# Kernel optimization log

Hardware: AMD Instinct MI355X
Metric: run time of the kernel (lower is better)

The kernel has to match this reference:

```python
import jax, jax.numpy as jnp
import numpy as np

B, N, F, L, H, C = 128, 512, 128, 64, 128, 10

def setup_inputs() -> dict:
    key = jax.random.key(0)
    ks = jax.random.split(key, 20)
    s = 0.1
    return {
        "g": jax.random.uniform(ks[0], (B, N, N), dtype=jnp.float32) + 1e-3,
        "h": jax.random.normal(ks[1], (B, N, F), dtype=jnp.float32),
        "labels": jax.random.randint(ks[2], (B,), 0, C),
        "eps": jax.random.normal(ks[3], (B, N, 1), dtype=jnp.float32),
        "W_s": jax.random.normal(ks[4], (F, L), dtype=jnp.float32) * s,
        "b_s": jnp.zeros((L,), jnp.float32),
        "W_mu": jax.random.normal(ks[5], (L, 1), dtype=jnp.float32) * s,
        "b_mu": jnp.zeros((1,), jnp.float32),
        "W_lv": jax.random.normal(ks[6], (L, 1), dtype=jnp.float32) * s,
        "b_lv": jnp.zeros((1,), jnp.float32),
        "W_dec": jax.random.normal(ks[7], (1, L), dtype=jnp.float32) * s,
        "b_dec": jnp.zeros((L,), jnp.float32),
        "W1": jax.random.normal(ks[8], (L, H), dtype=jnp.float32) * s,
        "b1": jnp.zeros((H,), jnp.float32),
        "W2": jax.random.normal(ks[9], (H, C), dtype=jnp.float32) * s,
        "b2": jnp.zeros((C,), jnp.float32),
        "beta": jnp.array([50.0], jnp.float32),
    }

def _gcn(gn, x, W, b):
    # GCN layer: propagate then project then ELU activation (dropout = 0)
    return jax.nn.elu(jnp.einsum('bnm,bmf->bnf', gn, x) @ W + b)

def reference(g, h, labels, eps, W_s, b_s, W_mu, b_mu, W_lv, b_lv, W_dec, b_dec, W1, b1, W2, b2, beta):
    # norm_g: degrees = sum over dim 1; broadcast division normalizes COLUMNS
    # (torch g/degrees with degrees of shape [N] divides g[:, j] by degrees[j])
    deg = jnp.sum(g, axis=1)                      # [B, N]
    gn = g / deg[:, None, :]                      # column-normalized adjacency
    h1 = _gcn(gn, h, W_s, b_s)                    # [B, N, L]
    mu = _gcn(gn, h1, W_mu, b_mu)                 # [B, N, 1]
    lv = _gcn(gn, h1, W_lv, b_lv)                 # [B, N, 1]
    z = mu + eps * jnp.exp(0.5 * lv)              # reparameterize (training)
    v = jax.nn.sigmoid(beta[0] * z)               # [B, N, 1]
    d = _gcn(gn, v, W_dec, b_dec)                 # [B, N, L]
    hp = jnp.einsum('bnl,bn->bl', h1, v[..., 0])  # h.T @ v pooling -> [B, L]
    logits = jax.nn.log_softmax(jax.nn.elu(hp @ W1 + b1) @ W2 + b2, axis=1)
    nll = -jnp.mean(logits[jnp.arange(B), labels])
    mus = mu.reshape(-1, 1)
    lvs = lv.reshape(-1, 1)
    M = mus.shape[0]
    kl = (-0.5 / M) * jnp.mean(jnp.sum(1.0 + 2.0 * lvs - mus**2 - jnp.exp(lvs)**2, axis=1))
    mse = jnp.mean((h1 - d) ** 2)
    loss = nll + kl + mse
    acc = jnp.mean((jnp.argmax(logits, axis=1) == labels).astype(jnp.float32))
    return (loss, acc)
```

## Files before the change

kernel.cpp:

```cpp
#include <hip/hip_runtime.h>

#define B_  128
#define N_  512
#define F_  128
#define L_  64
#define H_  128
#define C_  10

typedef short  bf8_t  __attribute__((ext_vector_type(8)));
typedef float  f32x4  __attribute__((ext_vector_type(4)));
typedef unsigned short us8 __attribute__((ext_vector_type(8)));

static __device__ __forceinline__ unsigned short f2bf(float x) {
    union { float f; unsigned u; } c; c.f = x;
    unsigned r = (c.u + 0x7fffu + ((c.u >> 16) & 1u)) >> 16;
    return (unsigned short)r;
}
static __device__ __forceinline__ float bf2f(unsigned short s) {
    union { unsigned u; float f; } c; c.u = ((unsigned)s) << 16;
    return c.f;
}
static __device__ __forceinline__ float elu(float x) { return x > 0.f ? x : expm1f(x); }

#define OFF_DEGP   0
#define OFF_DEG    2097152
#define OFF_HPP    2162688
#define OFF_KLP    2228224
#define OFF_MSEP   2229248
#define OFF_V      2230272
#define OFF_LP     2295808
#define OFF_COR    2295936
#define OFF_TMUBF  2296064
#define OFF_TLVBF  2328832
#define OFF_WVBF   2361600
#define OFF_H1Q    2394368
#define OFF_GBF    4491520
#define OFF_UBFT   21268736
#define OFF_WSTBF  23365888

__global__ __launch_bounds__(256) void k1_deg(const float* __restrict__ g,
                                              const float* __restrict__ Ws,
                                              float* __restrict__ deg_part,
                                              unsigned short* __restrict__ gbf,
                                              unsigned short* __restrict__ WsTbf) {
    const int c8 = blockIdx.x, b = blockIdx.y;
    if (c8 == 0 && b == 0) {
        for (int i = threadIdx.x; i < F_ * L_; i += 256) {
            int l = i >> 7, f = i & 127;
            WsTbf[i] = f2bf(Ws[f * L_ + l]);
        }
    }
    const int w = threadIdx.x >> 6, lane = threadIdx.x & 63;
    const int r0 = c8 * 64 + w * 16;
    const float*    gp = g   + ((size_t)b * N_ + r0) * N_ + lane * 8;
    unsigned short* gq = gbf + ((size_t)b * N_ + r0) * N_ + lane * 8;
    float cs[8] = {};
    #pragma unroll 4
    for (int r = 0; r < 16; ++r) {
        float4 v0 = *reinterpret_cast<const float4*>(gp + (size_t)r * N_);
        float4 v1 = *reinterpret_cast<const float4*>(gp + (size_t)r * N_ + 4);
        cs[0] += v0.x; cs[1] += v0.y; cs[2] += v0.z; cs[3] += v0.w;
        cs[4] += v1.x; cs[5] += v1.y; cs[6] += v1.z; cs[7] += v1.w;
        us8 qv;
        qv[0] = f2bf(v0.x); qv[1] = f2bf(v0.y); qv[2] = f2bf(v0.z); qv[3] = f2bf(v0.w);
        qv[4] = f2bf(v1.x); qv[5] = f2bf(v1.y); qv[6] = f2bf(v1.z); qv[7] = f2bf(v1.w);
        *reinterpret_cast<us8*>(gq + (size_t)r * N_) = qv;
    }
    const int s = c8 * 4 + w;
    float* dp = deg_part + ((size_t)(b * 32 + s)) * N_ + lane * 8;
    *reinterpret_cast<float4*>(dp)     = make_float4(cs[0], cs[1], cs[2], cs[3]);
    *reinterpret_cast<float4*>(dp + 4) = make_float4(cs[4], cs[5], cs[6], cs[7]);
}

__global__ __launch_bounds__(256) void k2_u(const float* __restrict__ h,
                                            const unsigned short* __restrict__ WsTbf,
                                            const float* __restrict__ deg_part,
                                            float* __restrict__ deg,
                                            unsigned short* __restrict__ ubfT) {
    __shared__ float tile[64 * 65];
    __shared__ float sdeg[64];
    const int b    = blockIdx.y;
    const int m0   = blockIdx.x * 64;
    const int tid  = threadIdx.x;
    const int wave = tid >> 6, lane = tid & 63;
    const int ml = lane & 15, q = lane >> 4;
    const int row0 = wave * 16;

    if (tid < 64) {
        int j = m0 + tid;
        float s = 0.f;
        #pragma unroll
        for (int k = 0; k < 32; ++k) s += deg_part[(size_t)(b * 32 + k) * N_ + j];
        sdeg[tid] = s;
        deg[b * N_ + j] = s;
    }

    const float* A = h + (size_t)(b * N_ + m0 + row0 + ml) * F_ + q * 8;
    const unsigned short* Bb = WsTbf + ml * F_ + q * 8;

    f32x4 acc[4] = {};
    #pragma unroll
    for (int kk = 0; kk < F_; kk += 32) {
        float4 a0 = *reinterpret_cast<const float4*>(A + kk);
        float4 a1 = *reinterpret_cast<const float4*>(A + kk + 4);
        union { unsigned short s[8]; bf8_t v; } av;
        av.s[0] = f2bf(a0.x); av.s[1] = f2bf(a0.y); av.s[2] = f2bf(a0.z); av.s[3] = f2bf(a0.w);
        av.s[4] = f2bf(a1.x); av.s[5] = f2bf(a1.y); av.s[6] = f2bf(a1.z); av.s[7] = f2bf(a1.w);
        #pragma unroll
        for (int i = 0; i < 4; ++i) {
            bf8_t bv = *reinterpret_cast<const bf8_t*>(Bb + i * 16 * F_ + kk);
            acc[i] = __builtin_amdgcn_mfma_f32_16x16x32_bf16(av.v, bv, acc[i], 0, 0, 0);
        }
    }
    __syncthreads();
    #pragma unroll
    for (int i = 0; i < 4; ++i) {
        int col = i * 16 + ml;
        #pragma unroll
        for (int r = 0; r < 4; ++r) {
            int rl = row0 + 4 * q + r;
            tile[rl * 65 + col] = acc[i][r] / sdeg[rl];
        }
    }
    __syncthreads();
    for (int jj = 0; jj < 16; ++jj) {
        int ll = wave + jj * 4;
        ubfT[(size_t)(b * L_ + ll) * N_ + m0 + lane] = f2bf(tile[lane * 65 + ll]);
    }
}

__global__ __launch_bounds__(256) void k3_h1(const unsigned short* __restrict__ gbf,
                                             const unsigned short* __restrict__ ubfT,
                                             const float* __restrict__ b_s,
                                             const float* __restrict__ Wmu,
                                             const float* __restrict__ Wlv,
                                             const float* __restrict__ deg,
                                             unsigned short* __restrict__ h1q,
                                             unsigned short* __restrict__ tmubf,
                                             unsigned short* __restrict__ tlvbf) {
    const int b    = blockIdx.y;
    const int tid  = threadIdx.x;
    const int wave = tid >> 6, lane = tid & 63;
    const int row0 = blockIdx.x * 64 + wave * 16;
    const int ml = lane & 15, q = lane >> 4;

    const unsigned short* A  = gbf  + (size_t)(b * N_ + row0 + ml) * N_ + q * 8;
    const unsigned short* B0 = ubfT + (size_t)(b * L_ + ml) * N_ + q * 8;

    f32x4 acc[4] = {};
    #pragma unroll 4
    for (int k = 0; k < N_; k += 32) {
        bf8_t a = *reinterpret_cast<const bf8_t*>(A + k);
        #pragma unroll
        for (int i = 0; i < 4; ++i) {
            bf8_t bb = *reinterpret_cast<const bf8_t*>(B0 + (size_t)i * 16 * N_ + k);
            acc[i] = __builtin_amdgcn_mfma_f32_16x16x32_bf16(a, bb, acc[i], 0, 0, 0);
        }
    }
    float bsv[4], wm[4], wl[4];
    #pragma unroll
    for (int i = 0; i < 4; ++i) {
        int col = i * 16 + ml;
        bsv[i] = b_s[col]; wm[i] = Wmu[col]; wl[i] = Wlv[col];
    }
    #pragma unroll
    for (int r = 0; r < 4; ++r) {
        int row = row0 + 4 * q + r;
        float pm = 0.f, pl = 0.f;
        #pragma unroll
        for (int i = 0; i < 4; ++i) {
            float hv = elu(acc[i][r] + bsv[i]);
            h1q[(size_t)(b * N_ + row) * L_ + i * 16 + ml] = f2bf(hv);
            pm = fmaf(hv, wm[i], pm);
            pl = fmaf(hv, wl[i], pl);
        }
        #pragma unroll
        for (int o = 1; o < 16; o <<= 1) { pm += __shfl_xor(pm, o); pl += __shfl_xor(pl, o); }
        if (ml == 0) {
            float idg = 1.f / deg[b * N_ + row];
            tmubf[b * N_ + row] = f2bf(pm * idg);
            tlvbf[b * N_ + row] = f2bf(pl * idg);
        }
    }
}

__global__ __launch_bounds__(256) void k5_v(const unsigned short* __restrict__ gbf,
                                            const unsigned short* __restrict__ tmubf,
                                            const unsigned short* __restrict__ tlvbf,
                                            const float* __restrict__ eps, const float* __restrict__ deg,
                                            const float* __restrict__ bmu, const float* __restrict__ blv,
                                            const float* __restrict__ beta,
                                            float* __restrict__ vv, unsigned short* __restrict__ wvbf,
                                            float* __restrict__ kl_part) {
    __shared__ float kls[4];
    const int b = blockIdx.y;
    const int wave = threadIdx.x >> 6, lane = threadIdx.x & 63;
    const int ml = lane & 15, q = lane >> 4;
    const int n0 = (blockIdx.x * 4 + wave) * 16;

    const unsigned short* A  = gbf + (size_t)(b * N_ + n0 + ml) * N_ + q * 8;
    const unsigned short* Bp = ((ml & 1) ? tlvbf : tmubf) + (size_t)b * N_ + q * 8;

    f32x4 acc = {};
    #pragma unroll
    for (int k = 0; k < N_; k += 32) {
        bf8_t a  = *reinterpret_cast<const bf8_t*>(A + k);
        bf8_t bb = *reinterpret_cast<const bf8_t*>(Bp + k);
        acc = __builtin_amdgcn_mfma_f32_16x16x32_bf16(a, bb, acc, 0, 0, 0);
    }
    float alv4[4];
    #pragma unroll
    for (int r = 0; r < 4; ++r) alv4[r] = __shfl_xor(acc[r], 1);

    float klv = 0.f;
    if (ml == 0) {
        const float bmu0 = bmu[0], blv0 = blv[0], beta0 = beta[0];
        #pragma unroll
        for (int r = 0; r < 4; ++r) {
            int n = n0 + 4 * q + r;
            float mu = elu(acc[r] + bmu0);
            float lv = elu(alv4[r] + blv0);
            float z  = mu + eps[b * N_ + n] * expf(0.5f * lv);
            float vs = 1.f / (1.f + expf(-beta0 * z));
            vv[b * N_ + n]   = vs;
            wvbf[b * N_ + n] = f2bf(vs / deg[b * N_ + n]);
            float e = expf(lv);
            klv += 1.f + 2.f * lv - mu * mu - e * e;
        }
    }
    klv += __shfl_xor(klv, 16);
    klv += __shfl_xor(klv, 32);
    if (lane == 0) kls[wave] = klv;
    __syncthreads();
    if (threadIdx.x == 0)
        kl_part[b * 8 + blockIdx.x] = kls[0] + kls[1] + kls[2] + kls[3];
}

__global__ __launch_bounds__(256) void k6_dec(const unsigned short* __restrict__ gbf,
                                              const unsigned short* __restrict__ wvbf,
                                              const float* __restrict__ vv,
                                              const unsigned short* __restrict__ h1q,
                                              const float* __restrict__ Wdec, const float* __restrict__ bdec,
                                              float* __restrict__ hp_part, float* __restrict__ mse_part) {
    __shared__ float hps[4 * 64];
    __shared__ float mses[4];
    const int b = blockIdx.y;
    const int tid = threadIdx.x, wave = tid >> 6, lane = tid & 63;
    const int ml = lane & 15, q = lane >> 4;
    const int n0 = (blockIdx.x * 4 + wave) * 16;

    const unsigned short* A  = gbf  + (size_t)(b * N_ + n0 + ml) * N_ + q * 8;
    const unsigned short* Bp = wvbf + (size_t)b * N_ + q * 8;

    f32x4 acc = {};
    #pragma unroll
    for (int k = 0; k < N_; k += 32) {
        bf8_t a  = *reinterpret_cast<const bf8_t*>(A + k);
        bf8_t bb = *reinterpret_cast<const bf8_t*>(Bp + k);
        acc = __builtin_amdgcn_mfma_f32_16x16x32_bf16(a, bb, acc, 0, 0, 0);
    }
    float pbc[16];
    #pragma unroll
    for (int t = 0; t < 16; ++t) pbc[t] = __shfl(acc[t & 3], (t >> 2) << 4);

    const float wd = Wdec[lane], bd = bdec[lane];
    float hpl = 0.f, msep = 0.f;
    #pragma unroll 4
    for (int t = 0; t < 16; ++t) {
        int n = n0 + t;
        float dv  = elu(pbc[t] * wd + bd);
        float h1v = bf2f(h1q[(size_t)(b * N_ + n) * L_ + lane]);
        float diff = h1v - dv;
        msep = fmaf(diff, diff, msep);
        hpl  = fmaf(h1v, vv[b * N_ + n], hpl);
    }
    hps[wave * 64 + lane] = hpl;
    #pragma unroll
    for (int o = 32; o; o >>= 1) msep += __shfl_xor(msep, o);
    if (lane == 0) mses[wave] = msep;
    __syncthreads();
    if (tid < 64) {
        float s = hps[tid] + hps[64 + tid] + hps[128 + tid] + hps[192 + tid];
        hp_part[(size_t)blockIdx.x * (B_ * 64) + b * 64 + tid] = s;
    }
    if (tid == 0)
        mse_part[b * 8 + blockIdx.x] = mses[0] + mses[1] + mses[2] + mses[3];
}

__global__ __launch_bounds__(128) void k7a_head(const float* __restrict__ hp_part,
                                                const float* __restrict__ W1, const float* __restrict__ b1,
                                                const float* __restrict__ W2, const float* __restrict__ b2,
                                                const int* __restrict__ labels,
                                                float* __restrict__ lp, float* __restrict__ cor) {
    __shared__ float hps[64];
    __shared__ float acts[128];
    __shared__ float lgs[10];
    const int b = blockIdx.x, tid = threadIdx.x;
    if (tid < 64) {
        float s = 0.f;
        #pragma unroll
        for (int x = 0; x < 8; ++x) s += hp_part[(size_t)x * (B_ * 64) + b * 64 + tid];
        hps[tid] = s;
    }
    __syncthreads();
    float s0 = 0, s1 = 0, s2 = 0, s3 = 0;
    for (int l = 0; l < 64; l += 4) {
        s0 += hps[l]     * W1[(l)     * H_ + tid];
        s1 += hps[l + 1] * W1[(l + 1) * H_ + tid];
        s2 += hps[l + 2] * W1[(l + 2) * H_ + tid];
        s3 += hps[l + 3] * W1[(l + 3) * H_ + tid];
    }
    acts[tid] = elu((s0 + s1) + (s2 + s3) + b1[tid]);
    __syncthreads();
    if (tid < C_) {
        float lg = b2[tid];
        for (int hh = 0; hh < H_; ++hh) lg += acts[hh] * W2[hh * C_ + tid];
        lgs[tid] = lg;
    }
    __syncthreads();
    if (tid == 0) {
        float mx = lgs[0]; int am = 0;
        for (int c = 1; c < C_; ++c) if (lgs[c] > mx) { mx = lgs[c]; am = c; }
        float se = 0.f;
        for (int c = 0; c < C_; ++c) se += expf(lgs[c] - mx);
        int lbl = labels[b];
        lp[b]  = lgs[lbl] - mx - logf(se);
        cor[b] = (am == lbl) ? 1.f : 0.f;
    }
}

__global__ __launch_bounds__(128) void k7b_final(const float* __restrict__ lp, const float* __restrict__ cor,
                                                 const float* __restrict__ kl_part, const float* __restrict__ mse_part,
                                                 float* __restrict__ out) {
    __shared__ float r1[128], r2[128], r3[128], r4[128];
    int tid = threadIdx.x;
    r1[tid] = lp[tid]; r2[tid] = cor[tid];
    float k = 0.f, m = 0.f;
    #pragma unroll
    for (int i = 0; i < 8; ++i)  k += kl_part[tid + i * 128];
    #pragma unroll
    for (int i = 0; i < 8; ++i)  m += mse_part[tid + i * 128];
    r3[tid] = k; r4[tid] = m;
    __syncthreads();
    for (int o = 64; o; o >>= 1) {
        if (tid < o) { r1[tid] += r1[tid + o]; r2[tid] += r2[tid + o];
                       r3[tid] += r3[tid + o]; r4[tid] += r4[tid + o]; }
        __syncthreads();
    }
    if (tid == 0) {
        float nll = -r1[0] / (float)B_;
        float kl  = r3[0] * (-0.5f / (65536.f * 65536.f));
        float mse = r4[0] / (float)(B_ * N_ * L_);
        out[0] = nll + kl + mse;
        out[1] = r2[0] / (float)B_;
    }
}

extern "C" void kernel_launch(void* const* d_in, const int* in_sizes, int n_in,
                              void* d_out, int out_size, void* d_ws, size_t ws_size,
                              hipStream_t stream) {
    const float* g     = (const float*)d_in[0];
    const float* h     = (const float*)d_in[1];
    const int*   labels= (const int*)  d_in[2];
    const float* eps   = (const float*)d_in[3];
    const float* W_s   = (const float*)d_in[4];
    const float* b_s   = (const float*)d_in[5];
    const float* W_mu  = (const float*)d_in[6];
    const float* b_mu  = (const float*)d_in[7];
    const float* W_lv  = (const float*)d_in[8];
    const float* b_lv  = (const float*)d_in[9];
    const float* W_dec = (const float*)d_in[10];
    const float* b_dec = (const float*)d_in[11];
    const float* W1    = (const float*)d_in[12];
    const float* b1    = (const float*)d_in[13];
    const float* W2    = (const float*)d_in[14];
    const float* b2    = (const float*)d_in[15];
    const float* beta  = (const float*)d_in[16];

    float* ws = (float*)d_ws;
    float* deg_part = ws + OFF_DEGP;
    float* deg      = ws + OFF_DEG;
    float* hp_part  = ws + OFF_HPP;
    float* kl_part  = ws + OFF_KLP;
    float* mse_part = ws + OFF_MSEP;
    float* vv       = ws + OFF_V;
    float* lp       = ws + OFF_LP;
    float* cor      = ws + OFF_COR;
    unsigned short* tmubf = (unsigned short*)(ws + OFF_TMUBF);
    unsigned short* tlvbf = (unsigned short*)(ws + OFF_TLVBF);
    unsigned short* wvbf  = (unsigned short*)(ws + OFF_WVBF);
    unsigned short* h1q   = (unsigned short*)(ws + OFF_H1Q);
    unsigned short* gbf   = (unsigned short*)(ws + OFF_GBF);
    unsigned short* ubfT  = (unsigned short*)(ws + OFF_UBFT);
    unsigned short* WsTbf = (unsigned short*)(ws + OFF_WSTBF);

    k1_deg  <<<dim3(8, B_), 256, 0, stream>>>(g, W_s, deg_part, gbf, WsTbf);
    k2_u    <<<dim3(8, B_), 256, 0, stream>>>(h, WsTbf, deg_part, deg, ubfT);
    k3_h1   <<<dim3(8, B_), 256, 0, stream>>>(gbf, ubfT, b_s, W_mu, W_lv, deg, h1q, tmubf, tlvbf);
    k5_v    <<<dim3(8, B_), 256, 0, stream>>>(gbf, tmubf, tlvbf, eps, deg, b_mu, b_lv, beta, vv, wvbf, kl_part);
    k6_dec  <<<dim3(8, B_), 256, 0, stream>>>(gbf, wvbf, vv, h1q, W_dec, b_dec, hp_part, mse_part);
    k7a_head<<<B_, 128, 0, stream>>>(hp_part, W1, b1, W2, b2, labels, lp, cor);
    k7b_final<<<1, 128, 0, stream>>>(lp, cor, kl_part, mse_part, (float*)d_out);
}
```

Before: 342.0 us.

## Move h·W_s projection into degree kernel and fuse final reduction into head

An extra block per batch is added to the degree kernel. It converts W_s to bf16 in swizzled LDS and computes the fp32 h·W_s projection into a transposed workspace, so this work overlaps with the adjacency pass. The former u kernel becomes a light pass that applies the degree normalisation and converts to bf16. The final reduction kernel is folded into the head kernel with an atomic ticket, so the last block does the global reduction and one launch goes away. The costs are an fp32 intermediate round-trip through memory and a serialised 8-subtile MFMA loop in the extra block, which could lengthen the critical path of k1.

```diff
diff --git a/kernel.cpp b/kernel.cpp
--- a/kernel.cpp
+++ b/kernel.cpp
@@ -30,27 +30,70 @@
 #define OFF_V      2230272
 #define OFF_LP     2295808
 #define OFF_COR    2295936
-#define OFF_TMUBF  2296064
-#define OFF_TLVBF  2328832
-#define OFF_WVBF   2361600
-#define OFF_H1Q    2394368
-#define OFF_GBF    4491520
-#define OFF_UBFT   21268736
-#define OFF_WSTBF  23365888
+#define OFF_KLB    2296064
+#define OFF_MSEB   2296192
+#define OFF_TMUBF  2296320
+#define OFF_TLVBF  2329088
+#define OFF_WVBF   2361856
+#define OFF_H1Q    2394624
+#define OFF_GBF    4491776
+#define OFF_UBFT   21269000
+#define OFF_UBFT2  21269504
+#define OFF_HWT    23366656
+#define OFF_TICKET 27560960
 
 __global__ __launch_bounds__(256) void k1_deg(const float* __restrict__ g,
+                                              const float* __restrict__ h,
                                               const float* __restrict__ Ws,
                                               float* __restrict__ deg_part,
                                               unsigned short* __restrict__ gbf,
-                                              unsigned short* __restrict__ WsTbf) {
-    const int c8 = blockIdx.x, b = blockIdx.y;
-    if (c8 == 0 && b == 0) {
-        for (int i = threadIdx.x; i < F_ * L_; i += 256) {
+                                              float* __restrict__ hwT,
+                                              unsigned* __restrict__ ticket) {
+    __shared__ unsigned short wst[64 * 128];
+    const int b = blockIdx.y;
+    const int tid = threadIdx.x;
+    const int w = tid >> 6, lane = tid & 63;
+
+    if (blockIdx.x == 8) {
+        if (b == 0 && tid == 0) *ticket = 0u;
+        for (int i = tid; i < F_ * L_; i += 256) {
             int l = i >> 7, f = i & 127;
-            WsTbf[i] = f2bf(Ws[f * L_ + l]);
-        }
-    }
-    const int w = threadIdx.x >> 6, lane = threadIdx.x & 63;
+            wst[l * F_ + (f ^ ((l & 7) << 3))] = f2bf(Ws[f * L_ + l]);
+        }
+        __syncthreads();
+        const int ml = lane & 15, q = lane >> 4;
+        for (int sub = 0; sub < 8; ++sub) {
+            const int m0 = (sub * 4 + w) * 16;
+            const float* Bp = h + (size_t)(b * N_ + m0 + ml) * F_ + q * 8;
+            f32x4 acc[4] = {};
+            #pragma unroll
+            for (int kk = 0; kk < F_; kk += 32) {
+                float4 b0 = *reinterpret_cast<const float4*>(Bp + kk);
+                float4 b1 = *reinterpret_cast<const float4*>(Bp + kk + 4);
+                union { unsigned short s[8]; bf8_t v; } bv;
+                bv.s[0] = f2bf(b0.x); bv.s[1] = f2bf(b0.y); bv.s[2] = f2bf(b0.z); bv.s[3] = f2bf(b0.w);
+                bv.s[4] = f2bf(b1.x); bv.s[5] = f2bf(b1.y); bv.s[6] = f2bf(b1.z); bv.s[7] = f2bf(b1.w);
+                #pragma unroll
+                for (int i = 0; i < 4; ++i) {
+                    const int l = i * 16 + ml;
+                    bf8_t av = *reinterpret_cast<const bf8_t*>(
+                        wst + l * F_ + ((q * 8 + kk) ^ ((ml & 7) << 3)));
+                    acc[i] = __builtin_amdgcn_mfma_f32_16x16x32_bf16(av, bv.v, acc[i], 0, 0, 0);
+                }
+            }
+            #pragma unroll
+            for (int i = 0; i < 4; ++i) {
+                #pragma unroll
+                for (int r = 0; r < 4; ++r) {
+                    int l = i * 16 + 4 * q + r;
+                    hwT[(size_t)(b * L_ + l) * N_ + m0 + ml] = acc[i][r];
+                }
+            }
+        }
+        return;
+    }
+
+    const int c8 = blockIdx.x;
     const int r0 = c8 * 64 + w * 16;
     const float*    gp = g   + ((size_t)b * N_ + r0) * N_ + lane * 8;
     unsigned short* gq = gbf + ((size_t)b * N_ + r0) * N_ + lane * 8;
@@ -72,61 +115,26 @@
     *reinterpret_cast<float4*>(dp + 4) = make_float4(cs[4], cs[5], cs[6], cs[7]);
 }
 
-__global__ __launch_bounds__(256) void k2_u(const float* __restrict__ h,
-                                            const unsigned short* __restrict__ WsTbf,
-                                            const float* __restrict__ deg_part,
-                                            float* __restrict__ deg,
-                                            unsigned short* __restrict__ ubfT) {
-    __shared__ float tile[64 * 65];
+__global__ __launch_bounds__(256) void k2p(const float* __restrict__ deg_part,
+                                           const float* __restrict__ hwT,
+                                           float* __restrict__ deg,
+                                           unsigned short* __restrict__ ubfT) {
     __shared__ float sdeg[64];
-    const int b    = blockIdx.y;
-    const int m0   = blockIdx.x * 64;
-    const int tid  = threadIdx.x;
-    const int wave = tid >> 6, lane = tid & 63;
-    const int ml = lane & 15, q = lane >> 4;
-    const int row0 = wave * 16;
-
+    const int b = blockIdx.y, mc = blockIdx.x, tid = threadIdx.x;
     if (tid < 64) {
-        int j = m0 + tid;
+        int col = mc * 64 + tid;
         float s = 0.f;
         #pragma unroll
-        for (int k = 0; k < 32; ++k) s += deg_part[(size_t)(b * 32 + k) * N_ + j];
+        for (int k = 0; k < 32; ++k) s += deg_part[(size_t)(b * 32 + k) * N_ + col];
         sdeg[tid] = s;
-        deg[b * N_ + j] = s;
-    }
-
-    const float* A = h + (size_t)(b * N_ + m0 + row0 + ml) * F_ + q * 8;
-    const unsigned short* Bb = WsTbf + ml * F_ + q * 8;
-
-    f32x4 acc[4] = {};
-    #pragma unroll
-    for (int kk = 0; kk < F_; kk += 32) {
-        float4 a0 = *reinterpret_cast<const float4*>(A + kk);
-        float4 a1 = *reinterpret_cast<const float4*>(A + kk + 4);
-        union { unsigned short s[8]; bf8_t v; } av;
-        av.s[0] = f2bf(a0.x); av.s[1] = f2bf(a0.y); av.s[2] = f2bf(a0.z); av.s[3] = f2bf(a0.w);
-        av.s[4] = f2bf(a1.x); av.s[5] = f2bf(a1.y); av.s[6] = f2bf(a1.z); av.s[7] = f2bf(a1.w);
-        #pragma unroll
-        for (int i = 0; i < 4; ++i) {
-            bf8_t bv = *reinterpret_cast<const bf8_t*>(Bb + i * 16 * F_ + kk);
-            acc[i] = __builtin_amdgcn_mfma_f32_16x16x32_bf16(av.v, bv, acc[i], 0, 0, 0);
-        }
-    }
-    __syncthreads();
-    #pragma unroll
-    for (int i = 0; i < 4; ++i) {
-        int col = i * 16 + ml;
-        #pragma unroll
-        for (int r = 0; r < 4; ++r) {
-            int rl = row0 + 4 * q + r;
-            tile[rl * 65 + col] = acc[i][r] / sdeg[rl];
-        }
-    }
-    __syncthreads();
-    for (int jj = 0; jj < 16; ++jj) {
-        int ll = wave + jj * 4;
-        ubfT[(size_t)(b * L_ + ll) * N_ + m0 + lane] = f2bf(tile[lane * 65 + ll]);
-    }
+        deg[b * N_ + col] = s;
+    }
+    __syncthreads();
+    const int m = mc * 64 + (tid & 63);
+    const float idg = 1.f / sdeg[tid & 63];
+    #pragma unroll
+    for (int l = tid >> 6; l < 64; l += 4)
+        ubfT[(size_t)(b * L_ + l) * N_ + m] = f2bf(hwT[(size_t)(b * L_ + l) * N_ + m] * idg);
 }
 
 __global__ __launch_bounds__(256) void k3_h1(const unsigned short* __restrict__ gbf,
@@ -287,14 +295,18 @@
         mse_part[b * 8 + blockIdx.x] = mses[0] + mses[1] + mses[2] + mses[3];
 }
 
-__global__ __launch_bounds__(128) void k7a_head(const float* __restrict__ hp_part,
-                                                const float* __restrict__ W1, const float* __restrict__ b1,
-                                                const float* __restrict__ W2, const float* __restrict__ b2,
-                                                const int* __restrict__ labels,
-                                                float* __restrict__ lp, float* __restrict__ cor) {
+__global__ __launch_bounds__(128) void k7_head(const float* __restrict__ hp_part,
+                                               const float* __restrict__ W1, const float* __restrict__ b1,
+                                               const float* __restrict__ W2, const float* __restrict__ b2,
+                                               const int* __restrict__ labels,
+                                               const float* __restrict__ kl_part, const float* __restrict__ mse_part,
+                                               float* __restrict__ lp, float* __restrict__ cor,
+                                               float* __restrict__ klb, float* __restrict__ mseb,
+                                               unsigned* __restrict__ ticket, float* __restrict__ out) {
     __shared__ float hps[64];
     __shared__ float acts[128];
     __shared__ float lgs[10];
+    __shared__ unsigned sold;
     const int b = blockIdx.x, tid = threadIdx.x;
     if (tid < 64) {
         float s = 0.f;
@@ -327,32 +339,39 @@
         lp[b]  = lgs[lbl] - mx - logf(se);
         cor[b] = (am == lbl) ? 1.f : 0.f;
     }
-}
-
-__global__ __launch_bounds__(128) void k7b_final(const float* __restrict__ lp, const float* __restrict__ cor,
-                                                 const float* __restrict__ kl_part, const float* __restrict__ mse_part,
-                                                 float* __restrict__ out) {
-    __shared__ float r1[128], r2[128], r3[128], r4[128];
-    int tid = threadIdx.x;
-    r1[tid] = lp[tid]; r2[tid] = cor[tid];
-    float k = 0.f, m = 0.f;
-    #pragma unroll
-    for (int i = 0; i < 8; ++i)  k += kl_part[tid + i * 128];
-    #pragma unroll
-    for (int i = 0; i < 8; ++i)  m += mse_part[tid + i * 128];
-    r3[tid] = k; r4[tid] = m;
-    __syncthreads();
-    for (int o = 64; o; o >>= 1) {
-        if (tid < o) { r1[tid] += r1[tid + o]; r2[tid] += r2[tid + o];
-                       r3[tid] += r3[tid + o]; r4[tid] += r4[tid + o]; }
+    if (tid == 1) {
+        float kk = 0.f;
+        #pragma unroll
+        for (int c = 0; c < 8; ++c) kk += kl_part[b * 8 + c];
+        klb[b] = kk;
+    }
+    if (tid == 2) {
+        float mm = 0.f;
+        #pragma unroll
+        for (int c = 0; c < 8; ++c) mm += mse_part[b * 8 + c];
+        mseb[b] = mm;
+    }
+    if (tid < 3) __threadfence();
+    __syncthreads();
+    if (tid == 0) sold = atomicAdd(ticket, 1u);
+    __syncthreads();
+    if (sold == 127u) {
+        __threadfence();
+        __shared__ float r1[128], r2[128], r3[128], r4[128];
+        r1[tid] = lp[tid]; r2[tid] = cor[tid]; r3[tid] = klb[tid]; r4[tid] = mseb[tid];
         __syncthreads();
-    }
-    if (tid == 0) {
-        float nll = -r1[0] / (float)B_;
-        float kl  = r3[0] * (-0.5f / (65536.f * 65536.f));
-        float mse = r4[0] / (float)(B_ * N_ * L_);
-        out[0] = nll + kl + mse;
-        out[1] = r2[0] / (float)B_;
+        for (int o = 64; o; o >>= 1) {
+            if (tid < o) { r1[tid] += r1[tid + o]; r2[tid] += r2[tid + o];
+                           r3[tid] += r3[tid + o]; r4[tid] += r4[tid + o]; }
+            __syncthreads();
+        }
+        if (tid == 0) {
+            float nll = -r1[0] / (float)B_;
+            float kl  = r3[0] * (-0.5f / (65536.f * 65536.f));
+            float mse = r4[0] / (float)(B_ * N_ * L_);
+            out[0] = nll + kl + mse;
+            out[1] = r2[0] / (float)B_;
+        }
     }
 }
 
@@ -386,19 +405,22 @@
     float* vv       = ws + OFF_V;
     float* lp       = ws + OFF_LP;
     float* cor      = ws + OFF_COR;
+    float* klb      = ws + OFF_KLB;
+    float* mseb     = ws + OFF_MSEB;
+    float* hwT      = ws + OFF_HWT;
+    unsigned* ticket = (unsigned*)(ws + OFF_TICKET);
     unsigned short* tmubf = (unsigned short*)(ws + OFF_TMUBF);
     unsigned short* tlvbf = (unsigned short*)(ws + OFF_TLVBF);
     unsigned short* wvbf  = (unsigned short*)(ws + OFF_WVBF);
     unsigned short* h1q   = (unsigned short*)(ws + OFF_H1Q);
     unsigned short* gbf   = (unsigned short*)(ws + OFF_GBF);
-    unsigned short* ubfT  = (unsigned short*)(ws + OFF_UBFT);
-    unsigned short* WsTbf = (unsigned short*)(ws + OFF_WSTBF);
-
-    k1_deg  <<<dim3(8, B_), 256, 0, stream>>>(g, W_s, deg_part, gbf, WsTbf);
-    k2_u    <<<dim3(8, B_), 256, 0, stream>>>(h, WsTbf, deg_part, deg, ubfT);
-    k3_h1   <<<dim3(8, B_), 256, 0, stream>>>(gbf, ubfT, b_s, W_mu, W_lv, deg, h1q, tmubf, tlvbf);
-    k5_v    <<<dim3(8, B_), 256, 0, stream>>>(gbf, tmubf, tlvbf, eps, deg, b_mu, b_lv, beta, vv, wvbf, kl_part);
-    k6_dec  <<<dim3(8, B_), 256, 0, stream>>>(gbf, wvbf, vv, h1q, W_dec, b_dec, hp_part, mse_part);
-    k7a_head<<<B_, 128, 0, stream>>>(hp_part, W1, b1, W2, b2, labels, lp, cor);
-    k7b_final<<<1, 128, 0, stream>>>(lp, cor, kl_part, mse_part, (float*)d_out);
-}
+    unsigned short* ubfT  = (unsigned short*)(ws + OFF_UBFT2);
+
+    k1_deg <<<dim3(9, B_), 256, 0, stream>>>(g, h, W_s, deg_part, gbf, hwT, ticket);
+    k2p    <<<dim3(8, B_), 256, 0, stream>>>(deg_part, hwT, deg, ubfT);
+    k3_h1  <<<dim3(8, B_), 256, 0, stream>>>(gbf, ubfT, b_s, W_mu, W_lv, deg, h1q, tmubf, tlvbf);
+    k5_v   <<<dim3(8, B_), 256, 0, stream>>>(gbf, tmubf, tlvbf, eps, deg, b_mu, b_lv, beta, vv, wvbf, kl_part);
+    k6_dec <<<dim3(8, B_), 256, 0, stream>>>(gbf, wvbf, vv, h1q, W_dec, b_dec, hp_part, mse_part);
+    k7_head<<<B_, 128, 0, stream>>>(hp_part, W1, b1, W2, b2, labels, kl_part, mse_part,
+                                    lp, cor, klb, mseb, ticket, (float*)d_out);
+}
```

Result: slower. 364.0 us (+6.4%).
